# Optimization experiments

Hardware: AMD Instinct MI355X
Metric: run time of the kernel (lower is better)

## Reference

```python
import jax, jax.numpy as jnp
import numpy as np

NODE_FEAT = 200  # F.interpolate size in run_all_node
TOPN = 2         # StitchModel.topn


def _node_feats(img, mask, flow, n_inst, max_pix):
    """Vectorized run_all_node: per-instance gather, linear interp to NODE_FEAT,
    3x3 sign histogram of flow[:2], mean of flow[2]. mask holds labels 1..n_inst;
    max_pix is a static upper bound on pixels per instance."""
    flat = mask.reshape(-1) - 1                       # labels 0..N-1
    order = jnp.argsort(flat)                         # stable sort by label
    counts = jax.ops.segment_sum(jnp.ones_like(flat), flat, num_segments=n_inst)
    starts = jnp.concatenate([jnp.zeros((1,), counts.dtype), jnp.cumsum(counts)[:-1]])
    j = jnp.arange(max_pix)
    pos = starts[:, None] + jnp.minimum(j[None, :], counts[:, None] - 1)
    idx = order[pos]                                  # [N, max_pix] padded pixel indices
    valid = j[None, :] < counts[:, None]              # [N, max_pix]
    iv = img.reshape(-1)[idx]                         # instance intensity profiles
    fx = flow[0].reshape(-1)[idx]
    fy = flow[1].reshape(-1)[idx]
    fz = flow[2].reshape(-1)[idx]
    cf = counts.astype(img.dtype)
    zflow = jnp.where(valid, fz, 0).sum(1) / cf       # flows[-1][m].mean()

    def interp(v, L):                                 # torch linear interp, align_corners=False
        Lf = L.astype(img.dtype)
        p = jnp.clip((jnp.arange(NODE_FEAT, dtype=img.dtype) + 0.5) * (Lf / NODE_FEAT) - 0.5,
                     0.0, Lf - 1.0)
        i0 = jnp.floor(p).astype(jnp.int32)
        i1 = jnp.minimum(i0 + 1, L - 1)
        w = p - i0.astype(img.dtype)
        return v[i0] * (1 - w) + v[i1] * w

    nodes = jax.vmap(interp)(iv, counts)              # [N, 200]
    # hist_flow_vector: bins ordered (x:<0,==0,>0) x (y:<0,==0,>0) -> 3*cx+cy
    cx = jnp.where(fx < 0, 0, jnp.where(fx == 0, 1, 2))
    cy = jnp.where(fy < 0, 0, jnp.where(fy == 0, 1, 2))
    bins = cx * 3 + cy
    oh = (bins[..., None] == jnp.arange(9)) & valid[..., None]
    hist = oh.sum(1).astype(img.dtype)                # [N, 9]
    return jnp.concatenate([nodes, hist], -1), zflow


def setup_inputs() -> dict:
    H = W = 2048
    N = 4096
    pix = (H * W) // N
    key = jax.random.key(0)
    ks = jax.random.split(key, 8)

    def make_mask(k):
        labels = (jnp.arange(H * W, dtype=jnp.int32) // pix) + 1   # labels 1..N
        perm = jax.random.permutation(k, H * W)
        return labels[perm].reshape(H, W)

    def make_bbox(k):
        u = jax.random.uniform(k, (N, 4), jnp.float32)
        centers = u[:, :2] * H
        sizes = u[:, 2:] * 49.0 + 1.0                               # nonzero w/h (asserted)
        return jnp.concatenate([centers, sizes], -1)

    return {
        "img1": jax.random.normal(ks[0], (H, W), jnp.float32),
        "img2": jax.random.normal(ks[1], (H, W), jnp.float32),
        "flow1": jax.random.normal(ks[2], (3, H, W), jnp.float32),
        "flow2": jax.random.normal(ks[3], (3, H, W), jnp.float32),
        "bbox1": make_bbox(ks[4]),
        "bbox2": make_bbox(ks[5]),
        "mask1": make_mask(ks[6]),
        "mask2": make_mask(ks[7]),
    }


def reference(img1, img2, flow1, flow2, bbox1, bbox2, mask1, mask2):
    N1, N2 = bbox1.shape[0], bbox2.shape[0]
    max1 = mask1.size // N1   # static bound on pixels/instance (equal-partition masks)
    max2 = mask2.size // N2
    node1, zf1 = _node_feats(img1, mask1, flow1, N1, max1)
    node2, zf2 = _node_feats(img2, mask2, flow2, N2, max2)
    x = jnp.concatenate([node1, node2], 0)            # [(N1+N2), 209]
    # build_one_graph_low_ram: per row, TOPN smallest center distances
    d = jnp.sqrt(((bbox1[:, None, :2] - bbox2[None, :, :2]) ** 2).sum(-1))  # [N1,N2]
    _, nbr = jax.lax.top_k(-d, TOPN)                  # smallest-first, like argsort[:topn]
    src = jnp.repeat(jnp.arange(N1), TOPN)            # [N1*TOPN]
    dst = nbr.reshape(-1)
    edge_index = jnp.stack([src, dst + N1])           # [2, N1*TOPN]
    edge_attr = jnp.stack([
        zf1[src], zf2[dst],
        bbox1[src, 0] - bbox2[dst, 0],
        bbox1[src, 1] - bbox2[dst, 1],
        bbox1[src, 2] / bbox2[dst, 2],
        bbox1[src, 3] / bbox2[dst, 3],
    ], -1)                                            # [N1*TOPN, 6]
    return x, edge_index, edge_attr
```

## Files before the change

### kernel.cpp

```cpp
#include <hip/hip_runtime.h>
#include <math.h>

#pragma clang fp contract(off)

#define HW      (2048*2048)
#define NI      4096
#define MAXPIX  1024
#define NF      200
#define FEAT    209
#define NE      (NI*2)
#define XSIZE   ((2*NI)*FEAT)
#define EIOFF   XSIZE
#define EAOFF   (EIOFF + 2*NE)

#define S       8192
#define CHK     (HW/S)
#define TOTCHK  (2*CHK)
#define NBPI    256
#define LPB     16
#define NBG     (2*NBPI)
#define REC     (2*HW)
#define BTOT    (LPB*MAXPIX)
#define NWS     16
#define NXCD    8

template<int NB>
__device__ __forceinline__ unsigned long long match_bits(int v) {
    unsigned long long m = ~0ull;
    #pragma unroll
    for (int bit = 0; bit < NB; ++bit) {
        unsigned long long bb = __ballot((v >> bit) & 1);
        m &= ((v >> bit) & 1) ? bb : ~bb;
    }
    return m;
}

__global__ void __launch_bounds__(512) count_zf_kernel(const int* __restrict__ mask1,
        const int* __restrict__ mask2, const float* __restrict__ flow1,
        const float* __restrict__ flow2, unsigned* __restrict__ cntA,
        float* __restrict__ zfpart) {
    __shared__ unsigned cnt[8][NBPI];
    __shared__ float zfp[NI];
    int t = threadIdx.x, w = t >> 6, lane = t & 63;
    for (int j = t; j < 8*NBPI; j += 512) ((unsigned*)cnt)[j] = 0u;
    for (int j = t; j < NI; j += 512) zfp[j] = 0.f;
    __syncthreads();
    int c = blockIdx.x;
    int img = c / CHK;
    const int4*   mask  = (const int4*)(img ? mask2 : mask1);
    const float4* flowz = (const float4*)((img ? flow2 : flow1) + 2L*HW);
    long base4 = (long)(c - img*CHK) * (S/4) + (long)w * (S/32);
    #pragma unroll
    for (int it = 0; it < S/32; it += 64) {
        int4   l4 = mask[base4 + it + lane];
        float4 fz = flowz[base4 + it + lane];
        atomicAdd(&cnt[w][(l4.x-1) >> 4], 1u);
        atomicAdd(&cnt[w][(l4.y-1) >> 4], 1u);
        atomicAdd(&cnt[w][(l4.z-1) >> 4], 1u);
        atomicAdd(&cnt[w][(l4.w-1) >> 4], 1u);
        atomicAdd(&zfp[l4.x-1], fz.x);
        atomicAdd(&zfp[l4.y-1], fz.y);
        atomicAdd(&zfp[l4.z-1], fz.z);
        atomicAdd(&zfp[l4.w-1], fz.w);
    }
    __syncthreads();
    if (t < NBPI) {
        unsigned s = 0;
        #pragma unroll
        for (int q = 0; q < 8; ++q) s += cnt[q][t];
        cntA[(long)c * NBPI + t] = s;
    }
    float* zdst = zfpart + (long)c * NI;
    for (int j = t; j < NI; j += 512) zdst[j] = zfp[j];
}

__global__ void __launch_bounds__(512) scan_kernel(unsigned* __restrict__ cntA) {
    __shared__ int wsum[8];
    int b = blockIdx.x;
    int img = b >> 8, lb = b & (NBPI - 1);
    int t = threadIdx.x, lane = t & 63, w = t >> 6;
    unsigned e = cntA[((long)img*CHK + t)*NBPI + lb];
    int incl = (int)e;
    #pragma unroll
    for (int off = 1; off < 64; off <<= 1) {
        int o = __shfl_up(incl, off);
        if (lane >= off) incl += o;
    }
    if (lane == 63) wsum[w] = incl;
    __syncthreads();
    int add = 0;
    for (int q = 0; q < w; ++q) add += wsum[q];
    cntA[((long)img*CHK + t)*NBPI + lb] = (unsigned)(incl + add - (int)e);
}

__global__ void __launch_bounds__(1024, 8) sort_kernel(
        const float* __restrict__ img1, const float* __restrict__ img2,
        const float* __restrict__ flow1, const float* __restrict__ flow2,
        const int* __restrict__ mask1, const int* __restrict__ mask2,
        const unsigned* __restrict__ cntA,
        float* __restrict__ riv, unsigned char* __restrict__ rmeta) {
    __shared__ float ivs[S];
    __shared__ unsigned short smeta[S];
    __shared__ unsigned short cw[NWS][NBPI];
    int* wsum  = (int*)smeta;
    int* gofsA = (int*)cw;
    int t = threadIdx.x, w = t >> 6, lane = t & 63;
    int bid = blockIdx.x;
    int c = (bid & (NXCD-1)) * (TOTCHK/NXCD) + (bid >> 3);
    int img = c / CHK;
    const int*   mask  = img ? mask2  : mask1;
    const float* image = img ? img2   : img1;
    const float* flow  = img ? flow2  : flow1;
    long base = (long)(c - img*CHK) * S;
    unsigned pre = 0;
    if (t < NBPI) pre = cntA[(long)c * NBPI + t];
    for (int j = t; j < NWS*NBPI; j += 1024) ((unsigned short*)cw)[j] = 0;
    {
        const int4*   mk = (const int4*)mask;
        const float4* iv = (const float4*)image;
        const float4* fx = (const float4*)flow;
        const float4* fy = (const float4*)(flow + HW);
        long i0 = (base >> 2) + (long)w*128 + lane;
        long i1 = i0 + 64;
        int4   m0 = mk[i0], m1 = mk[i1];
        float4 v0 = iv[i0], v1 = iv[i1];
        float4 x0 = fx[i0], x1 = fx[i1];
        float4 y0 = fy[i0], y1 = fy[i1];
        int p0 = (w<<9) + (lane<<2);
        ushort4 s0, s1;
        s0.x = (unsigned short)((m0.x-1) | (((x0.x<0.f?0:(x0.x==0.f?1:2))*3 + (y0.x<0.f?0:(y0.x==0.f?1:2))) << 12));
        s0.y = (unsigned short)((m0.y-1) | (((x0.y<0.f?0:(x0.y==0.f?1:2))*3 + (y0.y<0.f?0:(y0.y==0.f?1:2))) << 12));
        s0.z = (unsigned short)((m0.z-1) | (((x0.z<0.f?0:(x0.z==0.f?1:2))*3 + (y0.z<0.f?0:(y0.z==0.f?1:2))) << 12));
        s0.w = (unsigned short)((m0.w-1) | (((x0.w<0.f?0:(x0.w==0.f?1:2))*3 + (y0.w<0.f?0:(y0.w==0.f?1:2))) << 12));
        s1.x = (unsigned short)((m1.x-1) | (((x1.x<0.f?0:(x1.x==0.f?1:2))*3 + (y1.x<0.f?0:(y1.x==0.f?1:2))) << 12));
        s1.y = (unsigned short)((m1.y-1) | (((x1.y<0.f?0:(x1.y==0.f?1:2))*3 + (y1.y<0.f?0:(y1.y==0.f?1:2))) << 12));
        s1.z = (unsigned short)((m1.z-1) | (((x1.z<0.f?0:(x1.z==0.f?1:2))*3 + (y1.z<0.f?0:(y1.z==0.f?1:2))) << 12));
        s1.w = (unsigned short)((m1.w-1) | (((x1.w<0.f?0:(x1.w==0.f?1:2))*3 + (y1.w<0.f?0:(y1.w==0.f?1:2))) << 12));
        *(float4*)&ivs[p0]         = v0;
        *(float4*)&ivs[p0 + 256]   = v1;
        *(ushort4*)&smeta[p0]       = s0;
        *(ushort4*)&smeta[p0 + 256] = s1;
    }
    __syncthreads();
    int   pk[8];
    float piv[8];
    unsigned long long ltmask = (1ull << lane) - 1ull;
    #pragma unroll
    for (int it = 0; it < 8; ++it) {
        int p = (w<<9) + (it<<6) + lane;
        float ivx = ivs[p];
        int mt = (int)smeta[p];
        int bkt = (mt & 4095) >> 4;
        unsigned long long m = match_bits<8>(bkt);
        int cb = __popcll(m & ltmask);
        int ct = __popcll(m);
        piv[it] = ivx;
        pk[it] = (mt & 0xFFFF) | (cb << 16) | (ct << 22);
        if (cb == 0) cw[w][bkt] += (unsigned short)ct;
    }
    __syncthreads();
    int tot = 0, incl = 0;
    if (t < NBPI) {
        #pragma unroll
        for (int q = 0; q < NWS; ++q) tot += cw[q][t];
        incl = tot;
        #pragma unroll
        for (int off = 1; off < 64; off <<= 1) {
            int o = __shfl_up(incl, off);
            if (lane >= off) incl += o;
        }
        if (lane == 63) wsum[w] = incl;
    }
    __syncthreads();
    int gof = 0;
    if (t < NBPI) {
        int add = 0;
        for (int q = 0; q < w; ++q) add += wsum[q];
        int excl = incl + add - tot;
        int run = excl;
        #pragma unroll
        for (int q = 0; q < NWS; ++q) {
            int cq = cw[q][t];
            cw[q][t] = (unsigned short)run;
            run += cq;
        }
        gof = (img*NBPI + t) * BTOT + (int)pre - excl;
    }
    __syncthreads();
    #pragma unroll
    for (int it = 0; it < 8; ++it) {
        int pkv = pk[it];
        int l = pkv & 4095, bin = (pkv >> 12) & 15;
        int cb = (pkv >> 16) & 63, ct = (pkv >> 22) & 127;
        int bkt = l >> 4;
        int r0 = (int)cw[w][bkt];
        int dst = r0 + cb;
        if (cb == ct - 1) cw[w][bkt] = (unsigned short)(r0 + ct);
        ivs[dst] = piv[it];
        smeta[dst] = (unsigned short)((bkt << 8) | (bin << 4) | (l & 15));
    }
    __syncthreads();
    if (t < NBPI) gofsA[t] = gof;
    __syncthreads();
    for (int j = t; j < S; j += 1024) {
        int ms = (int)smeta[j];
        int b = ms >> 8;
        int g = gofsA[b] + j;
        riv[g]   = ivs[j];
        rmeta[g] = (unsigned char)(ms & 0xFF);
    }
}

__global__ void __launch_bounds__(1024) stageB_kernel(
        const float* __restrict__ riv, const unsigned char* __restrict__ rmeta,
        const float* __restrict__ zfpart, float* __restrict__ out,
        float* __restrict__ zfm) {
    __shared__ float acc[LPB * NF];
    __shared__ float s_tw[MAXPIX];
    __shared__ int   s_tk[MAXPIX];
    __shared__ int   hist[LPB * 9];
    __shared__ int   qc[16][LPB];
    __shared__ int   cur[16][LPB];
    __shared__ float red[16][64];
    int t = threadIdx.x, w = t >> 6, lane = t & 63;
    int b = blockIdx.x;
    if (b >= NBG) {
        int b2 = b - NBG;
        int img = b2 >> 6;
        int l0  = (b2 & 63) * 64;
        const float* p = zfpart + ((long)img*CHK + w)*NI + l0 + lane;
        float s = 0.f;
        #pragma unroll 8
        for (int r = 0; r < CHK; r += 16) s += p[(long)r*NI];
        red[w][lane] = s;
        __syncthreads();
        if (t < 64) {
            float sum = 0.f;
            #pragma unroll
            for (int g = 0; g < 16; ++g) sum += red[g][t];
            zfm[img*NI + l0 + t] = sum * (1.0f/(float)MAXPIX);
        }
        return;
    }
    for (int j = t; j < LPB*NF; j += 1024) acc[j] = 0.f;
    if (t < MAXPIX) s_tk[t] = -1;
    if (t < LPB*9) hist[t] = 0;
    if (t < 16*LPB) ((int*)qc)[t] = 0;
    __syncthreads();
    if (t < NF) {
        const float Lf = (float)MAXPIX;
        float p = ((float)t + 0.5f) * (Lf / (float)NF) - 0.5f;
        p = fminf(fmaxf(p, 0.0f), Lf - 1.0f);
        int i0 = (int)floorf(p);
        int i1 = min(i0 + 1, MAXPIX - 1);
        float wg = p - (float)i0;
        s_tk[i0] = t; s_tw[i0] = 1.0f - wg;
        s_tk[i1] = t; s_tw[i1] = wg;
    }
    long base = (long)b * BTOT;
    const int qsz = BTOT / 16;
    int qbeg = w * qsz;
    unsigned long long ltmask = (1ull << lane) - 1ull;
    {
        const uchar4* rm4 = (const uchar4*)(rmeta + base + qbeg);
        #pragma unroll
        for (int it = 0; it < 4; ++it) {
            uchar4 m = rm4[it*64 + lane];
            int l0 = m.x & 15, l1 = m.y & 15, l2 = m.z & 15, l3 = m.w & 15;
            unsigned long long mm;
            mm = match_bits<4>(l0); if ((mm & ltmask) == 0) qc[w][l0] += __popcll(mm);
            mm = match_bits<4>(l1); if ((mm & ltmask) == 0) qc[w][l1] += __popcll(mm);
            mm = match_bits<4>(l2); if ((mm & ltmask) == 0) qc[w][l2] += __popcll(mm);
            mm = match_bits<4>(l3); if ((mm & ltmask) == 0) qc[w][l3] += __popcll(mm);
        }
    }
    __syncthreads();
    if (t < LPB) {
        int s = 0;
        #pragma unroll
        for (int q = 0; q < 16; ++q) { cur[q][t] = s; s += qc[q][t]; }
    }
    __syncthreads();
    #pragma unroll
    for (int it = 0; it < 16; ++it) {
        int i = qbeg + it*64 + lane;
        int meta = (int)rmeta[base + i];
        float iv = riv[base + i];
        int ll = meta & 15;
        unsigned long long mll = ~0ull, m8;
        #pragma unroll
        for (int bit = 0; bit < 4; ++bit) {
            unsigned long long bb = __ballot((meta >> bit) & 1);
            mll &= ((meta >> bit) & 1) ? bb : ~bb;
        }
        m8 = mll;
        #pragma unroll
        for (int bit = 4; bit < 8; ++bit) {
            unsigned long long bb = __ballot((meta >> bit) & 1);
            m8 &= ((meta >> bit) & 1) ? bb : ~bb;
        }
        int cb = __popcll(mll & ltmask);
        int ct = __popcll(mll);
        int r0 = cur[w][ll];
        int rank = r0 + cb;
        if (cb == ct - 1) cur[w][ll] = r0 + ct;
        if ((m8 & ltmask) == 0)
            atomicAdd(&hist[ll*9 + (meta >> 4)], __popcll(m8));
        int k = s_tk[rank];
        if (k >= 0) atomicAdd(&acc[ll*NF + k], iv * s_tw[rank]);
    }
    __syncthreads();
    for (int j = t; j < LPB*FEAT; j += 1024) {
        int r = j / FEAT, k = j - r*FEAT;
        float v = (k < NF) ? acc[r*NF + k] : (float)hist[r*9 + (k - NF)];
        out[(long)b * LPB * FEAT + j] = v;
    }
}

__device__ __forceinline__ bool better(float d, int j, float d2, int j2) {
    return d < d2 || (d == d2 && j < j2);
}

__global__ void __launch_bounds__(256) edge_kernel(const float* __restrict__ bbox1,
                                                   const float* __restrict__ bbox2,
                                                   const float* __restrict__ zfm,
                                                   float* __restrict__ out) {
    __shared__ float sbx[NI], sby[NI];
    int wave = threadIdx.x >> 6, lane = threadIdx.x & 63;
    for (int r = threadIdx.x; r < NI; r += 256) {
        float4 b = ((const float4*)bbox2)[r];
        sbx[r] = b.x; sby[r] = b.y;
    }
    __syncthreads();
    int i = blockIdx.x * 4 + wave;
    float c1x = bbox1[i*4 + 0], c1y = bbox1[i*4 + 1];
    float d0 = INFINITY; int j0 = 0x7fffffff;
    float d1 = INFINITY; int j1 = 0x7fffffff;
    for (int t = 0; t < NI; t += 64) {
        int j = t + lane;
        float dx = c1x - sbx[j];
        float dy = c1y - sby[j];
        float dsq = dx*dx + dy*dy;
        float d = (float)sqrt((double)dsq);
        if (better(d, j, d0, j0)) { d1 = d0; j1 = j0; d0 = d; j0 = j; }
        else if (better(d, j, d1, j1)) { d1 = d; j1 = j; }
    }
    for (int off = 32; off; off >>= 1) {
        float od0 = __shfl_down(d0, off); int oj0 = __shfl_down(j0, off);
        float od1 = __shfl_down(d1, off); int oj1 = __shfl_down(j1, off);
        if (better(od0, oj0, d0, j0)) {
            if (better(d0, j0, od1, oj1)) { d1 = d0; j1 = j0; }
            else                          { d1 = od1; j1 = oj1; }
            d0 = od0; j0 = oj0;
        } else if (better(od0, oj0, d1, j1)) { d1 = od0; j1 = oj0; }
    }
    if (lane == 0) {
        float z1 = zfm[i];
        int js[2] = { j0, j1 };
        for (int t = 0; t < 2; ++t) {
            int e = i*2 + t, j = js[t];
            out[EIOFF + e]      = (float)i;
            out[EIOFF + NE + e] = (float)(j + NI);
            float* ea = out + EAOFF + (long)e * 6;
            ea[0] = z1;
            ea[1] = zfm[NI + j];
            ea[2] = c1x - bbox2[j*4 + 0];
            ea[3] = c1y - bbox2[j*4 + 1];
            ea[4] = bbox1[i*4 + 2] / bbox2[j*4 + 2];
            ea[5] = bbox1[i*4 + 3] / bbox2[j*4 + 3];
        }
    }
}

extern "C" void kernel_launch(void* const* d_in, const int* in_sizes, int n_in,
                              void* d_out, int out_size, void* d_ws, size_t ws_size,
                              hipStream_t stream) {
    const float* img1  = (const float*)d_in[0];
    const float* img2  = (const float*)d_in[1];
    const float* flow1 = (const float*)d_in[2];
    const float* flow2 = (const float*)d_in[3];
    const float* bbox1 = (const float*)d_in[4];
    const float* bbox2 = (const float*)d_in[5];
    const int*   mask1 = (const int*)d_in[6];
    const int*   mask2 = (const int*)d_in[7];
    float* out = (float*)d_out;

    char* ws = (char*)d_ws;
    size_t off = 0;
    unsigned* cntA   = (unsigned*)(ws + off); off += (size_t)TOTCHK * NBPI * 4;
    float*    riv    = (float*)(ws + off);    off += (size_t)REC * 4;
    float*    zfpart = (float*)(ws + off);    off += (size_t)TOTCHK * NI * 4;
    float*    zfm    = (float*)(ws + off);    off += 2 * NI * 4;
    unsigned char* rmeta = (unsigned char*)(ws + off); off += (size_t)REC;

    hipLaunchKernelGGL(count_zf_kernel, dim3(TOTCHK), dim3(512), 0, stream,
                       mask1, mask2, flow1, flow2, cntA, zfpart);
    hipLaunchKernelGGL(scan_kernel, dim3(NBG), dim3(512), 0, stream, cntA);
    hipLaunchKernelGGL(sort_kernel, dim3(TOTCHK), dim3(1024), 0, stream,
                       img1, img2, flow1, flow2, mask1, mask2, cntA, riv, rmeta);
    hipLaunchKernelGGL(stageB_kernel, dim3(NBG + 128), dim3(1024), 0, stream,
                       riv, rmeta, zfpart, out, zfm);
    hipLaunchKernelGGL(edge_kernel, dim3(NI/4), dim3(256), 0, stream,
                       bbox1, bbox2, zfm, out);
}
```

Baseline: 299.2 us.

## Merge count blocks pairwise, restructure scan, simplify stageB histogram ballots

The count kernel now handles two chunks per 1024-thread block, which halves the zfpart partial rows that stageB must reduce. The scan kernel is rewritten to 32 blocks, each scanning 16 buckets across all chunk rows with multi-pass carry propagation, replacing 512 small blocks. StageB drops the 8-bit ballot match for the histogram and uses plain per-lane shared atomics, and the sort kernel keeps gofs in its own shared array to remove one barrier. The costs are more shared-atomic contention in the histogram and fewer, more serialized scan blocks.

Measured after the change: 302.6 us. Within noise of the previous version (+1.1%).

```diff
diff --git a/kernel.cpp b/kernel.cpp
--- a/kernel.cpp
+++ b/kernel.cpp
@@ -23,6 +23,7 @@
 #define BTOT    (LPB*MAXPIX)
 #define NWS     16
 #define NXCD    8
+#define ZROWS   512
 
 template<int NB>
 __device__ __forceinline__ unsigned long long match_bits(int v) {
@@ -35,21 +36,22 @@
     return m;
 }
 
-__global__ void __launch_bounds__(512) count_zf_kernel(const int* __restrict__ mask1,
+__global__ void __launch_bounds__(1024) count_zf_kernel(const int* __restrict__ mask1,
         const int* __restrict__ mask2, const float* __restrict__ flow1,
         const float* __restrict__ flow2, unsigned* __restrict__ cntA,
         float* __restrict__ zfpart) {
-    __shared__ unsigned cnt[8][NBPI];
+    __shared__ unsigned cnt[16][NBPI];
     __shared__ float zfp[NI];
     int t = threadIdx.x, w = t >> 6, lane = t & 63;
-    for (int j = t; j < 8*NBPI; j += 512) ((unsigned*)cnt)[j] = 0u;
-    for (int j = t; j < NI; j += 512) zfp[j] = 0.f;
-    __syncthreads();
-    int c = blockIdx.x;
-    int img = c / CHK;
+    for (int j = t; j < 16*NBPI; j += 1024) ((unsigned*)cnt)[j] = 0u;
+    for (int j = t; j < NI; j += 1024) zfp[j] = 0.f;
+    __syncthreads();
+    int c0 = blockIdx.x * 2;
+    int img = c0 / CHK;
+    int c = c0 + (w >> 3);
     const int4*   mask  = (const int4*)(img ? mask2 : mask1);
     const float4* flowz = (const float4*)((img ? flow2 : flow1) + 2L*HW);
-    long base4 = (long)(c - img*CHK) * (S/4) + (long)w * (S/32);
+    long base4 = (long)(c - img*CHK) * (S/4) + (long)(w & 7) * (S/32);
     #pragma unroll
     for (int it = 0; it < S/32; it += 64) {
         int4   l4 = mask[base4 + it + lane];
@@ -64,33 +66,51 @@
         atomicAdd(&zfp[l4.w-1], fz.w);
     }
     __syncthreads();
-    if (t < NBPI) {
+    if (t < 2*NBPI) {
+        int cc = c0 + (t >> 8), b = t & (NBPI - 1);
+        int r0 = (t >> 8) * 8;
         unsigned s = 0;
         #pragma unroll
-        for (int q = 0; q < 8; ++q) s += cnt[q][t];
-        cntA[(long)c * NBPI + t] = s;
-    }
-    float* zdst = zfpart + (long)c * NI;
-    for (int j = t; j < NI; j += 512) zdst[j] = zfp[j];
-}
-
-__global__ void __launch_bounds__(512) scan_kernel(unsigned* __restrict__ cntA) {
-    __shared__ int wsum[8];
+        for (int q = 0; q < 8; ++q) s += cnt[r0 + q][b];
+        cntA[(long)cc * NBPI + b] = s;
+    }
+    float* zdst = zfpart + (long)blockIdx.x * NI;
+    for (int j = t; j < NI; j += 1024) zdst[j] = zfp[j];
+}
+
+#define SCB 16
+__global__ void __launch_bounds__(1024) scan_kernel(unsigned* __restrict__ cntA) {
+    __shared__ int wsum[16][SCB];
+    __shared__ int pbase[SCB];
+    int t = threadIdx.x, w = t >> 6, lane = t & 63;
     int b = blockIdx.x;
-    int img = b >> 8, lb = b & (NBPI - 1);
-    int t = threadIdx.x, lane = t & 63, w = t >> 6;
-    unsigned e = cntA[((long)img*CHK + t)*NBPI + lb];
-    int incl = (int)e;
-    #pragma unroll
-    for (int off = 1; off < 64; off <<= 1) {
-        int o = __shfl_up(incl, off);
-        if (lane >= off) incl += o;
-    }
-    if (lane == 63) wsum[w] = incl;
-    __syncthreads();
-    int add = 0;
-    for (int q = 0; q < w; ++q) add += wsum[q];
-    cntA[((long)img*CHK + t)*NBPI + lb] = (unsigned)(incl + add - (int)e);
+    int img = b >> 4;
+    int b0 = (b & 15) * SCB;
+    int bk = lane & 15, r4 = lane >> 4;
+    if (t < SCB) pbase[t] = 0;
+    __syncthreads();
+    for (int pass = 0; pass < 8; ++pass) {
+        int row = pass*64 + w*4 + r4;
+        long idx = ((long)img*CHK + row)*NBPI + b0 + bk;
+        unsigned e = cntA[idx];
+        int incl = (int)e, o;
+        o = __shfl_up(incl, 16); if (lane >= 16) incl += o;
+        o = __shfl_up(incl, 32); if (lane >= 32) incl += o;
+        if (lane >= 48) wsum[w][bk] = incl;
+        __syncthreads();
+        int add = pbase[bk];
+        #pragma unroll
+        for (int q = 0; q < 16; ++q) if (q < w) add += wsum[q][bk];
+        cntA[idx] = (unsigned)(incl + add - (int)e);
+        __syncthreads();
+        if (t < SCB) {
+            int s = 0;
+            #pragma unroll
+            for (int q = 0; q < 16; ++q) s += wsum[q][t];
+            pbase[t] += s;
+        }
+        __syncthreads();
+    }
 }
 
 __global__ void __launch_bounds__(1024, 8) sort_kernel(
@@ -102,8 +122,8 @@
     __shared__ float ivs[S];
     __shared__ unsigned short smeta[S];
     __shared__ unsigned short cw[NWS][NBPI];
-    int* wsum  = (int*)smeta;
-    int* gofsA = (int*)cw;
+    __shared__ int gofs[NBPI];
+    int* wsum = (int*)smeta;
     int t = threadIdx.x, w = t >> 6, lane = t & 63;
     int bid = blockIdx.x;
     int c = (bid & (NXCD-1)) * (TOTCHK/NXCD) + (bid >> 3);
@@ -172,7 +192,6 @@
         if (lane == 63) wsum[w] = incl;
     }
     __syncthreads();
-    int gof = 0;
     if (t < NBPI) {
         int add = 0;
         for (int q = 0; q < w; ++q) add += wsum[q];
@@ -184,7 +203,7 @@
             cw[q][t] = (unsigned short)run;
             run += cq;
         }
-        gof = (img*NBPI + t) * BTOT + (int)pre - excl;
+        gofs[t] = (img*NBPI + t) * BTOT + (int)pre - excl;
     }
     __syncthreads();
     #pragma unroll
@@ -200,12 +219,10 @@
         smeta[dst] = (unsigned short)((bkt << 8) | (bin << 4) | (l & 15));
     }
     __syncthreads();
-    if (t < NBPI) gofsA[t] = gof;
-    __syncthreads();
     for (int j = t; j < S; j += 1024) {
         int ms = (int)smeta[j];
         int b = ms >> 8;
-        int g = gofsA[b] + j;
+        int g = gofs[b] + j;
         riv[g]   = ivs[j];
         rmeta[g] = (unsigned char)(ms & 0xFF);
     }
@@ -228,10 +245,10 @@
         int b2 = b - NBG;
         int img = b2 >> 6;
         int l0  = (b2 & 63) * 64;
-        const float* p = zfpart + ((long)img*CHK + w)*NI + l0 + lane;
+        const float* p = zfpart + ((long)img*(ZROWS/2) + w)*NI + l0 + lane;
         float s = 0.f;
-        #pragma unroll 8
-        for (int r = 0; r < CHK; r += 16) s += p[(long)r*NI];
+        #pragma unroll
+        for (int r = 0; r < ZROWS/2; r += 16) s += p[(long)r*NI];
         red[w][lane] = s;
         __syncthreads();
         if (t < 64) {
@@ -287,25 +304,13 @@
         int meta = (int)rmeta[base + i];
         float iv = riv[base + i];
         int ll = meta & 15;
-        unsigned long long mll = ~0ull, m8;
-        #pragma unroll
-        for (int bit = 0; bit < 4; ++bit) {
-            unsigned long long bb = __ballot((meta >> bit) & 1);
-            mll &= ((meta >> bit) & 1) ? bb : ~bb;
-        }
-        m8 = mll;
-        #pragma unroll
-        for (int bit = 4; bit < 8; ++bit) {
-            unsigned long long bb = __ballot((meta >> bit) & 1);
-            m8 &= ((meta >> bit) & 1) ? bb : ~bb;
-        }
+        unsigned long long mll = match_bits<4>(ll);
         int cb = __popcll(mll & ltmask);
         int ct = __popcll(mll);
         int r0 = cur[w][ll];
         int rank = r0 + cb;
         if (cb == ct - 1) cur[w][ll] = r0 + ct;
-        if ((m8 & ltmask) == 0)
-            atomicAdd(&hist[ll*9 + (meta >> 4)], __popcll(m8));
+        atomicAdd(&hist[ll*9 + (meta >> 4)], 1);
         int k = s_tk[rank];
         if (k >= 0) atomicAdd(&acc[ll*NF + k], iv * s_tw[rank]);
     }
@@ -389,13 +394,13 @@
     size_t off = 0;
     unsigned* cntA   = (unsigned*)(ws + off); off += (size_t)TOTCHK * NBPI * 4;
     float*    riv    = (float*)(ws + off);    off += (size_t)REC * 4;
-    float*    zfpart = (float*)(ws + off);    off += (size_t)TOTCHK * NI * 4;
+    float*    zfpart = (float*)(ws + off);    off += (size_t)ZROWS * NI * 4;
     float*    zfm    = (float*)(ws + off);    off += 2 * NI * 4;
     unsigned char* rmeta = (unsigned char*)(ws + off); off += (size_t)REC;
 
-    hipLaunchKernelGGL(count_zf_kernel, dim3(TOTCHK), dim3(512), 0, stream,
+    hipLaunchKernelGGL(count_zf_kernel, dim3(TOTCHK/2), dim3(1024), 0, stream,
                        mask1, mask2, flow1, flow2, cntA, zfpart);
-    hipLaunchKernelGGL(scan_kernel, dim3(NBG), dim3(512), 0, stream, cntA);
+    hipLaunchKernelGGL(scan_kernel, dim3(32), dim3(1024), 0, stream, cntA);
     hipLaunchKernelGGL(sort_kernel, dim3(TOTCHK), dim3(1024), 0, stream,
                        img1, img2, flow1, flow2, mask1, mask2, cntA, riv, rmeta);
     hipLaunchKernelGGL(stageB_kernel, dim3(NBG + 128), dim3(1024), 0, stream,
```
